# Kernel optimization log

Hardware: AMD Instinct MI355X
Metric: run time of the kernel (lower is better)

## Reference

```python
import jax, jax.numpy as jnp
import numpy as np

B, T, D, HS = 32, 2048, 384, 64

def setup_inputs() -> dict:
    key = jax.random.key(0)
    kx, kq, kk, kv = jax.random.split(key, 4)
    x = jax.random.normal(kx, (B, T, D), dtype=jnp.float32)
    s = 1.0 / np.sqrt(D)  # Linear-like init scale
    Wq = jax.random.normal(kq, (D, HS), dtype=jnp.float32) * s
    Wk = jax.random.normal(kk, (D, HS), dtype=jnp.float32) * s
    Wv = jax.random.normal(kv, (D, HS), dtype=jnp.float32) * s
    return {"x": x, "Wq": Wq, "Wk": Wk, "Wv": Wv}

def reference(x, Wq, Wk, Wv):
    # Single-head causal self-attention (dropout in eval mode -> identity).
    Tlen = x.shape[1]
    q = x @ Wq  # [B,T,HS]
    k = x @ Wk
    v = x @ Wv
    scale = q.shape[-1] ** (-0.5)
    wei = jnp.einsum('bqd,bkd->bqk', q, k) * scale  # [B,T,T]
    causal = jnp.tril(jnp.ones((Tlen, Tlen), dtype=bool))
    wei = jnp.where(causal, wei, jnp.finfo(wei.dtype).min)
    wei = jax.nn.softmax(wei, axis=-1)
    return jnp.einsum('bqk,bkd->bqd', wei, v)  # [B,T,HS]
```

## Files before the change

kernel.cpp:

```cpp
#include <hip/hip_runtime.h>
#include <hip/hip_bf16.h>

#define T_LEN 2048
#define NBATCH 32

typedef __bf16 bf16x8 __attribute__((ext_vector_type(8)));
typedef float f32x4 __attribute__((ext_vector_type(4)));

__device__ __forceinline__ unsigned short f2bf(float f) {
  return __builtin_bit_cast(unsigned short, __float2bfloat16(f));
}
__device__ __forceinline__ unsigned int pk2(float a, float b) {
  return (unsigned int)f2bf(a) | ((unsigned int)f2bf(b) << 16);
}
__device__ __forceinline__ bf16x8 ld16(const void* p) {
  return __builtin_bit_cast(bf16x8, *(const uint4*)p);
}
__device__ __forceinline__ void gl_lds16(const void* g, void* l) {
  __builtin_amdgcn_global_load_lds(
      (const __attribute__((address_space(1))) unsigned int*)g,
      (__attribute__((address_space(3))) unsigned int*)l, 16, 0, 0);
}

__global__ __launch_bounds__(256) void k_wprep(const float* __restrict__ Wq,
                                               const float* __restrict__ Wk,
                                               const float* __restrict__ Wv,
                                               unsigned short* __restrict__ Wt3) {
  int idx = blockIdx.x * 256 + threadIdx.x;
  if (idx >= 192 * 384) return;
  int c = idx / 384;
  int k = idx % 384;
  const float* W = (c < 64) ? Wq : ((c < 128) ? Wk : Wv);
  Wt3[idx] = f2bf(W[k * 64 + (c & 63)]);
}

__global__ __launch_bounds__(256) void k_proj(const float* __restrict__ x,
                                              const unsigned short* __restrict__ Wt3,
                                              unsigned short* __restrict__ Qb,
                                              unsigned short* __restrict__ Kb,
                                              unsigned short* __restrict__ VTb) {
  __shared__ __align__(16) unsigned short xs[128 * 32];
  __shared__ __align__(16) unsigned short wt[192 * 32];
  const int tid = threadIdx.x;
  const int lane = tid & 63, w = tid >> 6;
  const int g = lane >> 4, lr = lane & 15;
  const long row0 = (long)blockIdx.x * 128;

  f32x4 acc[2][12] = {};

  for (int ks = 0; ks < 12; ++ks) {
    const int k0 = ks * 32;
    __syncthreads();
    {
      int r = tid >> 1, c0 = (tid & 1) * 16;
      const float4* src = reinterpret_cast<const float4*>(&x[(row0 + r) * 384 + k0 + c0]);
      float4 f0 = src[0], f1 = src[1], f2 = src[2], f3 = src[3];
      uint4 u0, u1;
      u0.x = pk2(f0.x, f0.y); u0.y = pk2(f0.z, f0.w);
      u0.z = pk2(f1.x, f1.y); u0.w = pk2(f1.z, f1.w);
      u1.x = pk2(f2.x, f2.y); u1.y = pk2(f2.z, f2.w);
      u1.z = pk2(f3.x, f3.y); u1.w = pk2(f3.z, f3.w);
      int b0 = (r * 64 + c0 * 2) ^ ((r & 7) << 4);
      int b1 = (r * 64 + c0 * 2 + 16) ^ ((r & 7) << 4);
      *reinterpret_cast<uint4*>((char*)xs + b0) = u0;
      *reinterpret_cast<uint4*>((char*)xs + b1) = u1;
    }
#pragma unroll
    for (int j = 0; j < 3; ++j) {
      int chunk = tid + 256 * j;
      int r = chunk >> 2, c8 = chunk & 3;
      uint4 d = *reinterpret_cast<const uint4*>(&Wt3[r * 384 + k0 + c8 * 8]);
      int b = (r * 64 + c8 * 16) ^ ((r & 7) << 4);
      *reinterpret_cast<uint4*>((char*)wt + b) = d;
    }
    __syncthreads();

    bf16x8 a[2];
#pragma unroll
    for (int mt = 0; mt < 2; ++mt) {
      int r = w * 32 + mt * 16 + lr;
      a[mt] = ld16((char*)xs + ((r * 64 + g * 16) ^ ((r & 7) << 4)));
    }
#pragma unroll
    for (int n = 0; n < 12; ++n) {
      int r = n * 16 + lr;
      bf16x8 bb = ld16((char*)wt + ((r * 64 + g * 16) ^ ((r & 7) << 4)));
      acc[0][n] = __builtin_amdgcn_mfma_f32_16x16x32_bf16(a[0], bb, acc[0][n], 0, 0, 0);
      acc[1][n] = __builtin_amdgcn_mfma_f32_16x16x32_bf16(a[1], bb, acc[1][n], 0, 0, 0);
    }
  }

#pragma unroll
  for (int mt = 0; mt < 2; ++mt)
#pragma unroll
    for (int n = 0; n < 12; ++n)
#pragma unroll
      for (int rr = 0; rr < 4; ++rr) {
        long grow = row0 + w * 32 + mt * 16 + g * 4 + rr;
        int col = n * 16 + lr;
        unsigned short hv = f2bf(acc[mt][n][rr]);
        if (n < 4) {
          Qb[grow * 64 + col] = hv;
        } else if (n < 8) {
          Kb[grow * 64 + (col - 64)] = hv;
        } else {
          long bb_ = grow >> 11;
          long t = grow & 2047;
          VTb[(bb_ * 64 + (col - 128)) * 2048 + t] = hv;
        }
      }
}

__global__ __launch_bounds__(256, 4) void k_attn(const unsigned short* __restrict__ Qb,
                                                 const unsigned short* __restrict__ Kb,
                                                 const unsigned short* __restrict__ VTb,
                                                 float* __restrict__ out) {
  __shared__ __align__(16) char ksm[2 * 8192];
  __shared__ __align__(16) char vsm[2 * 8192];
  __shared__ __align__(16) unsigned short psm[4 * 16 * 64];

  const int tid = threadIdx.x;
  const int lane = tid & 63, w = tid >> 6;
  const int g = lane >> 4, lr = lane & 15;
  const int b = blockIdx.x;
  const int qt = (gridDim.y - 1) - blockIdx.y;
  const int qrow0 = qt * 64 + w * 16;

  const char* Kg = (const char*)(Kb + (long)b * T_LEN * 64);
  const char* Vg = (const char*)(VTb + (long)b * 64 * 2048);

  const int lrow = lane >> 3;
  const int lsw = (((lane & 7) ^ lrow) << 4);

  bf16x8 qf[2];
#pragma unroll
  for (int c = 0; c < 2; ++c)
    qf[c] = ld16(&Qb[((long)(b * T_LEN + qrow0 + lr)) * 64 + c * 32 + g * 8]);

  f32x4 o[4] = {};
  float m_r[4], l_r[4];
#pragma unroll
  for (int r = 0; r < 4; ++r) { m_r[r] = -1e30f; l_r[r] = 0.f; }

  char* pbase = (char*)psm + w * 2048;
  const int nkv = qt + 1;

  {
    const char* gk = Kg + ((long)(0 + w * 16 + lrow)) * 128 + lsw;
    const char* gv = Vg + ((long)(w * 16 + lrow)) * 4096 + lsw;
    char* kb = ksm + w * 2048;
    char* vb = vsm + w * 2048;
    gl_lds16(gk, kb);             gl_lds16(gk + 8 * 128, kb + 1024);
    gl_lds16(gv, vb);             gl_lds16(gv + 8 * 4096, vb + 1024);
  }
  __syncthreads();

  int cur = 0;
  for (int t = 0; t < nkv; ++t) {
    const int kv0 = t * 64;

    if (t + 1 < nkv) {
      const int kv1 = kv0 + 64;
      const char* gk = Kg + ((long)(kv1 + w * 16 + lrow)) * 128 + lsw;
      const char* gv = Vg + ((long)(w * 16 + lrow)) * 4096 + (long)kv1 * 2 + lsw;
      char* kb = ksm + (cur ^ 1) * 8192 + w * 2048;
      char* vb = vsm + (cur ^ 1) * 8192 + w * 2048;
      gl_lds16(gk, kb);           gl_lds16(gk + 8 * 128, kb + 1024);
      gl_lds16(gv, vb);           gl_lds16(gv + 8 * 4096, vb + 1024);
    }

    char* kt = ksm + cur * 8192;
    char* vt = vsm + cur * 8192;

    f32x4 s[4] = {};
    __builtin_amdgcn_s_setprio(1);
#pragma unroll
    for (int c = 0; c < 2; ++c)
#pragma unroll
      for (int n = 0; n < 4; ++n) {
        int r = n * 16 + lr;
        bf16x8 kf = ld16(kt + ((r * 128 + c * 64 + g * 16) ^ ((r & 7) << 4)));
        s[n] = __builtin_amdgcn_mfma_f32_16x16x32_bf16(qf[c], kf, s[n], 0, 0, 0);
      }
    __builtin_amdgcn_s_setprio(0);

    const bool diag = (t == qt);
#pragma unroll
    for (int n = 0; n < 4; ++n)
#pragma unroll
      for (int r = 0; r < 4; ++r) {
        float v = s[n][r] * 0.125f;
        if (diag) {
          int col = kv0 + n * 16 + lr;
          int rowq = qrow0 + g * 4 + r;
          if (col > rowq) v = -1e30f;
        }
        s[n][r] = v;
      }

    float pm[4];
#pragma unroll
    for (int r = 0; r < 4; ++r)
      pm[r] = fmaxf(fmaxf(s[0][r], s[1][r]), fmaxf(s[2][r], s[3][r]));
    bool need = false;
#pragma unroll
    for (int r = 0; r < 4; ++r) need = need || (pm[r] > m_r[r] + 8.0f);
    if (__any((int)need)) {
#pragma unroll
      for (int r = 0; r < 4; ++r) {
        float mx = pm[r];
        mx = fmaxf(mx, __shfl_xor(mx, 1));
        mx = fmaxf(mx, __shfl_xor(mx, 2));
        mx = fmaxf(mx, __shfl_xor(mx, 4));
        mx = fmaxf(mx, __shfl_xor(mx, 8));
        float mn = fmaxf(m_r[r], mx);
        float sc = exp2f((m_r[r] - mn) * 1.44269504f);
        m_r[r] = mn;
        l_r[r] *= sc;
#pragma unroll
        for (int n = 0; n < 4; ++n) o[n][r] *= sc;
      }
    }
    float pr[4][4];
#pragma unroll
    for (int r = 0; r < 4; ++r)
#pragma unroll
      for (int n = 0; n < 4; ++n) {
        float p = exp2f((s[n][r] - m_r[r]) * 1.44269504f);
        pr[n][r] = p;
        l_r[r] += p;
      }

#pragma unroll
    for (int n = 0; n < 4; ++n)
#pragma unroll
      for (int r = 0; r < 4; ++r) {
        int rq = g * 4 + r;
        int col = n * 16 + lr;
        *(unsigned short*)(pbase + ((rq * 128 + col * 2) ^ ((rq & 7) << 4))) = f2bf(pr[n][r]);
      }

    bf16x8 pf[2];
#pragma unroll
    for (int c = 0; c < 2; ++c)
      pf[c] = ld16(pbase + ((lr * 128 + c * 64 + g * 16) ^ ((lr & 7) << 4)));
    __builtin_amdgcn_s_setprio(1);
#pragma unroll
    for (int c = 0; c < 2; ++c)
#pragma unroll
      for (int n = 0; n < 4; ++n) {
        int r = n * 16 + lr;
        bf16x8 vf = ld16(vt + ((r * 128 + c * 64 + g * 16) ^ ((r & 7) << 4)));
        o[n] = __builtin_amdgcn_mfma_f32_16x16x32_bf16(pf[c], vf, o[n], 0, 0, 0);
      }
    __builtin_amdgcn_s_setprio(0);

    __syncthreads();
    cur ^= 1;
  }

#pragma unroll
  for (int r = 0; r < 4; ++r) {
    float l = l_r[r];
    l += __shfl_xor(l, 1);
    l += __shfl_xor(l, 2);
    l += __shfl_xor(l, 4);
    l += __shfl_xor(l, 8);
    float inv = 1.0f / l;
#pragma unroll
    for (int n = 0; n < 4; ++n) {
      long rowg = (long)b * T_LEN + qrow0 + g * 4 + r;
      out[rowg * 64 + n * 16 + lr] = o[n][r] * inv;
    }
  }
}

extern "C" void kernel_launch(void* const* d_in, const int* in_sizes, int n_in,
                              void* d_out, int out_size, void* d_ws, size_t ws_size,
                              hipStream_t stream) {
  const float* x  = (const float*)d_in[0];
  const float* Wq = (const float*)d_in[1];
  const float* Wk = (const float*)d_in[2];
  const float* Wv = (const float*)d_in[3];
  float* out = (float*)d_out;

  char* ws = (char*)d_ws;
  unsigned short* Wt3 = (unsigned short*)ws;
  unsigned short* Qb  = (unsigned short*)(ws + 0x80000);
  unsigned short* Kb  = (unsigned short*)(ws + 0x80000 + 0x800000);
  unsigned short* VTb = (unsigned short*)(ws + 0x80000 + 0x1000000);

  k_wprep<<<dim3(288), dim3(256), 0, stream>>>(Wq, Wk, Wv, Wt3);
  k_proj<<<dim3(512), dim3(256), 0, stream>>>(x, Wt3, Qb, Kb, VTb);
  k_attn<<<dim3(NBATCH, 32), dim3(256), 0, stream>>>(Qb, Kb, VTb, out);
}
```

Measured before the change: 85.79 us.

## Rewrite attention with 32x32 MFMA, 128-row query tiles and register-only P

Switches the attention kernel from 16x16x32 to 32x32x16 bf16 MFMA and computes S transposed (K times Q), so each lane owns one query row. That row ownership removes most cross-lane softmax reductions. Each block now covers 128 query rows with 32 per wave, halving the grid and the K/V tile loads per query row. P is moved into the A-operand layout with lane shuffles instead of a round trip through shared memory, and fully masked tiles are skipped per wave. In exchange it needs more registers (occupancy hint drops to 2), fewer blocks to balance, and more imbalance between waves on diagonal tiles.

```diff
diff --git a/kernel.cpp b/kernel.cpp
--- a/kernel.cpp
+++ b/kernel.cpp
@@ -6,6 +6,7 @@
 
 typedef __bf16 bf16x8 __attribute__((ext_vector_type(8)));
 typedef float f32x4 __attribute__((ext_vector_type(4)));
+typedef float f32x16 __attribute__((ext_vector_type(16)));
 
 __device__ __forceinline__ unsigned short f2bf(float f) {
   return __builtin_bit_cast(unsigned short, __float2bfloat16(f));
@@ -111,20 +112,20 @@
       }
 }
 
-__global__ __launch_bounds__(256, 4) void k_attn(const unsigned short* __restrict__ Qb,
+__global__ __launch_bounds__(256, 2) void k_attn(const unsigned short* __restrict__ Qb,
                                                  const unsigned short* __restrict__ Kb,
                                                  const unsigned short* __restrict__ VTb,
                                                  float* __restrict__ out) {
   __shared__ __align__(16) char ksm[2 * 8192];
   __shared__ __align__(16) char vsm[2 * 8192];
-  __shared__ __align__(16) unsigned short psm[4 * 16 * 64];
 
   const int tid = threadIdx.x;
   const int lane = tid & 63, w = tid >> 6;
-  const int g = lane >> 4, lr = lane & 15;
+  const int h = lane >> 5, q31 = lane & 31;
   const int b = blockIdx.x;
-  const int qt = (gridDim.y - 1) - blockIdx.y;
-  const int qrow0 = qt * 64 + w * 16;
+  const int qb = (gridDim.y - 1) - blockIdx.y;
+  const int qw = qb * 128 + w * 32;
+  const int qrow = qw + q31;
 
   const char* Kg = (const char*)(Kb + (long)b * T_LEN * 64);
   const char* Vg = (const char*)(VTb + (long)b * 64 * 2048);
@@ -132,21 +133,18 @@
   const int lrow = lane >> 3;
   const int lsw = (((lane & 7) ^ lrow) << 4);
 
-  bf16x8 qf[2];
-#pragma unroll
-  for (int c = 0; c < 2; ++c)
-    qf[c] = ld16(&Qb[((long)(b * T_LEN + qrow0 + lr)) * 64 + c * 32 + g * 8]);
-
-  f32x4 o[4] = {};
-  float m_r[4], l_r[4];
-#pragma unroll
-  for (int r = 0; r < 4; ++r) { m_r[r] = -1e30f; l_r[r] = 0.f; }
-
-  char* pbase = (char*)psm + w * 2048;
-  const int nkv = qt + 1;
+  bf16x8 qf[4];
+#pragma unroll
+  for (int c = 0; c < 4; ++c)
+    qf[c] = ld16(&Qb[(long)(b * T_LEN + qrow) * 64 + c * 16 + h * 8]);
+
+  f32x16 o[2] = {};
+  float m_r = -1e30f, l_r = 0.f;
+
+  const int nkv = 2 * qb + 2;
 
   {
-    const char* gk = Kg + ((long)(0 + w * 16 + lrow)) * 128 + lsw;
+    const char* gk = Kg + ((long)(w * 16 + lrow)) * 128 + lsw;
     const char* gv = Vg + ((long)(w * 16 + lrow)) * 4096 + lsw;
     char* kb = ksm + w * 2048;
     char* vb = vsm + w * 2048;
@@ -172,106 +170,101 @@
     char* kt = ksm + cur * 8192;
     char* vt = vsm + cur * 8192;
 
-    f32x4 s[4] = {};
-    __builtin_amdgcn_s_setprio(1);
-#pragma unroll
-    for (int c = 0; c < 2; ++c)
-#pragma unroll
-      for (int n = 0; n < 4; ++n) {
-        int r = n * 16 + lr;
-        bf16x8 kf = ld16(kt + ((r * 128 + c * 64 + g * 16) ^ ((r & 7) << 4)));
-        s[n] = __builtin_amdgcn_mfma_f32_16x16x32_bf16(qf[c], kf, s[n], 0, 0, 0);
+    if (kv0 <= qw + 31) {
+      f32x16 s[2] = {};
+      __builtin_amdgcn_s_setprio(1);
+#pragma unroll
+      for (int mf = 0; mf < 2; ++mf)
+#pragma unroll
+        for (int c = 0; c < 4; ++c) {
+          int r = mf * 32 + q31;
+          bf16x8 kf = ld16(kt + r * 128 + ((c * 32 + h * 16) ^ ((r & 7) << 4)));
+          s[mf] = __builtin_amdgcn_mfma_f32_32x32x16_bf16(kf, qf[c], s[mf], 0, 0, 0);
+        }
+      __builtin_amdgcn_s_setprio(0);
+
+      const bool domask = (kv0 + 63 > qw);
+#pragma unroll
+      for (int mf = 0; mf < 2; ++mf)
+#pragma unroll
+        for (int r = 0; r < 16; ++r) {
+          float v = s[mf][r] * 0.125f;
+          if (domask) {
+            int kvv = kv0 + mf * 32 + (r & 3) + 8 * (r >> 2) + 4 * h;
+            if (kvv > qrow) v = -1e30f;
+          }
+          s[mf][r] = v;
+        }
+
+      float pm = -3e38f;
+#pragma unroll
+      for (int mf = 0; mf < 2; ++mf)
+#pragma unroll
+        for (int r = 0; r < 16; ++r) pm = fmaxf(pm, s[mf][r]);
+      if (__any(pm > m_r + 8.0f)) {
+        float mx = fmaxf(pm, __shfl_xor(pm, 32));
+        float mn = fmaxf(m_r, mx);
+        float sc = exp2f((m_r - mn) * 1.44269504f);
+        m_r = mn;
+        l_r *= sc;
+#pragma unroll
+        for (int r = 0; r < 16; ++r) {
+          int qp = (r & 3) + 8 * (r >> 2) + 4 * h;
+          float scq = __shfl(sc, qp);
+          o[0][r] *= scq;
+          o[1][r] *= scq;
+        }
       }
-    __builtin_amdgcn_s_setprio(0);
-
-    const bool diag = (t == qt);
-#pragma unroll
-    for (int n = 0; n < 4; ++n)
-#pragma unroll
-      for (int r = 0; r < 4; ++r) {
-        float v = s[n][r] * 0.125f;
-        if (diag) {
-          int col = kv0 + n * 16 + lr;
-          int rowq = qrow0 + g * 4 + r;
-          if (col > rowq) v = -1e30f;
-        }
-        s[n][r] = v;
+#pragma unroll
+      for (int mf = 0; mf < 2; ++mf)
+#pragma unroll
+        for (int r = 0; r < 16; ++r) {
+          float p = exp2f((s[mf][r] - m_r) * 1.44269504f);
+          s[mf][r] = p;
+          l_r += p;
+        }
+
+      __builtin_amdgcn_s_setprio(1);
+#pragma unroll
+      for (int c = 0; c < 4; ++c) {
+        const int mf = c >> 1, rb = (c & 1) * 8;
+        unsigned int lo0 = pk2(s[mf][rb + 0], s[mf][rb + 1]);
+        unsigned int lo1 = pk2(s[mf][rb + 2], s[mf][rb + 3]);
+        unsigned int hi0 = pk2(s[mf][rb + 4], s[mf][rb + 5]);
+        unsigned int hi1 = pk2(s[mf][rb + 6], s[mf][rb + 7]);
+        unsigned int sA = h ? lo0 : hi0;
+        unsigned int sB = h ? lo1 : hi1;
+        unsigned int rA = (unsigned int)__shfl_xor((int)sA, 32);
+        unsigned int rB = (unsigned int)__shfl_xor((int)sB, 32);
+        uint4 pw;
+        pw.x = h ? rA : lo0;
+        pw.y = h ? rB : lo1;
+        pw.z = h ? hi0 : rA;
+        pw.w = h ? hi1 : rB;
+        bf16x8 pf = __builtin_bit_cast(bf16x8, pw);
+#pragma unroll
+        for (int db = 0; db < 2; ++db) {
+          int rd = db * 32 + q31;
+          bf16x8 vf = ld16(vt + rd * 128 + ((c * 32 + h * 16) ^ ((rd & 7) << 4)));
+          o[db] = __builtin_amdgcn_mfma_f32_32x32x16_bf16(pf, vf, o[db], 0, 0, 0);
+        }
       }
-
-    float pm[4];
-#pragma unroll
-    for (int r = 0; r < 4; ++r)
-      pm[r] = fmaxf(fmaxf(s[0][r], s[1][r]), fmaxf(s[2][r], s[3][r]));
-    bool need = false;
-#pragma unroll
-    for (int r = 0; r < 4; ++r) need = need || (pm[r] > m_r[r] + 8.0f);
-    if (__any((int)need)) {
-#pragma unroll
-      for (int r = 0; r < 4; ++r) {
-        float mx = pm[r];
-        mx = fmaxf(mx, __shfl_xor(mx, 1));
-        mx = fmaxf(mx, __shfl_xor(mx, 2));
-        mx = fmaxf(mx, __shfl_xor(mx, 4));
-        mx = fmaxf(mx, __shfl_xor(mx, 8));
-        float mn = fmaxf(m_r[r], mx);
-        float sc = exp2f((m_r[r] - mn) * 1.44269504f);
-        m_r[r] = mn;
-        l_r[r] *= sc;
-#pragma unroll
-        for (int n = 0; n < 4; ++n) o[n][r] *= sc;
-      }
-    }
-    float pr[4][4];
-#pragma unroll
-    for (int r = 0; r < 4; ++r)
-#pragma unroll
-      for (int n = 0; n < 4; ++n) {
-        float p = exp2f((s[n][r] - m_r[r]) * 1.44269504f);
-        pr[n][r] = p;
-        l_r[r] += p;
-      }
-
-#pragma unroll
-    for (int n = 0; n < 4; ++n)
-#pragma unroll
-      for (int r = 0; r < 4; ++r) {
-        int rq = g * 4 + r;
-        int col = n * 16 + lr;
-        *(unsigned short*)(pbase + ((rq * 128 + col * 2) ^ ((rq & 7) << 4))) = f2bf(pr[n][r]);
-      }
-
-    bf16x8 pf[2];
-#pragma unroll
-    for (int c = 0; c < 2; ++c)
-      pf[c] = ld16(pbase + ((lr * 128 + c * 64 + g * 16) ^ ((lr & 7) << 4)));
-    __builtin_amdgcn_s_setprio(1);
-#pragma unroll
-    for (int c = 0; c < 2; ++c)
-#pragma unroll
-      for (int n = 0; n < 4; ++n) {
-        int r = n * 16 + lr;
-        bf16x8 vf = ld16(vt + ((r * 128 + c * 64 + g * 16) ^ ((r & 7) << 4)));
-        o[n] = __builtin_amdgcn_mfma_f32_16x16x32_bf16(pf[c], vf, o[n], 0, 0, 0);
-      }
-    __builtin_amdgcn_s_setprio(0);
+      __builtin_amdgcn_s_setprio(0);
+    }
 
     __syncthreads();
     cur ^= 1;
   }
 
-#pragma unroll
-  for (int r = 0; r < 4; ++r) {
-    float l = l_r[r];
-    l += __shfl_xor(l, 1);
-    l += __shfl_xor(l, 2);
-    l += __shfl_xor(l, 4);
-    l += __shfl_xor(l, 8);
-    float inv = 1.0f / l;
-#pragma unroll
-    for (int n = 0; n < 4; ++n) {
-      long rowg = (long)b * T_LEN + qrow0 + g * 4 + r;
-      out[rowg * 64 + n * 16 + lr] = o[n][r] * inv;
-    }
+  float lt = l_r + __shfl_xor(l_r, 32);
+  float linv = 1.0f / lt;
+#pragma unroll
+  for (int r = 0; r < 16; ++r) {
+    int qp = (r & 3) + 8 * (r >> 2) + 4 * h;
+    float iv = __shfl(linv, qp);
+    long rowg = (long)(b * T_LEN + qw + qp);
+    out[rowg * 64 + q31]      = o[0][r] * iv;
+    out[rowg * 64 + 32 + q31] = o[1][r] * iv;
   }
 }
 
@@ -292,5 +285,5 @@
 
   k_wprep<<<dim3(288), dim3(256), 0, stream>>>(Wq, Wk, Wv, Wt3);
   k_proj<<<dim3(512), dim3(256), 0, stream>>>(x, Wt3, Qb, Kb, VTb);
-  k_attn<<<dim3(NBATCH, 32), dim3(256), 0, stream>>>(Qb, Kb, VTb, out);
-}
+  k_attn<<<dim3(NBATCH, 16), dim3(256), 0, stream>>>(Qb, Kb, VTb, out);
+}
```

After: 117.2 us. 1.37x slower.
